# Performance work log

Hardware: AMD Instinct MI355X
Metric: run time of the kernel (lower is better)

## Reference

```python
import jax, jax.numpy as jnp
import numpy as np

B, S, D, H = 2, 2048, 1024, 16  # batch, seq, embed_dim, num_heads
DH = D // H                      # head dim = 64


def setup_inputs() -> dict:
    key = jax.random.key(0)
    kx, kq, kbq, kk, kbk, kv, kbv = jax.random.split(key, 7)
    scale = 1.0 / np.sqrt(D)
    return {
        "x": jax.random.normal(kx, (B, S, D), dtype=jnp.float32),
        "Wq": jax.random.normal(kq, (D, D), dtype=jnp.float32) * scale,
        "bq": jax.random.normal(kbq, (D,), dtype=jnp.float32) * 0.01,
        "Wk": jax.random.normal(kk, (D, D), dtype=jnp.float32) * scale,
        "bk": jax.random.normal(kbk, (D,), dtype=jnp.float32) * 0.01,
        "Wv": jax.random.normal(kv, (D, D), dtype=jnp.float32) * scale,
        "bv": jax.random.normal(kbv, (D,), dtype=jnp.float32) * 0.01,
    }


def reference(x, Wq, bq, Wk, bk, Wv, bv):
    # ooqkv_type == 'q', odeint_method == 'id': q branch = act(Linear(x)), exact GELU (torch nn.GELU default)
    q = jax.nn.gelu(x @ Wq + bq, approximate=False)
    k = x @ Wk + bk
    v = x @ Wv + bv
    # [B, S, D] -> [B, S, H, DH]
    q = q.reshape(B, S, H, DH)
    k = k.reshape(B, S, H, DH)
    v = v.reshape(B, S, H, DH)
    # NOTE: original module has NO 1/sqrt(d) scale — faithful reproduction
    att = jnp.einsum("bqhd,bkhd->bhqk", q, k)
    att = jax.nn.softmax(att, axis=-1)
    out = jnp.einsum("bhqk,bkhd->bqhd", att, v)
    return out.reshape(B, S, D)
```

## Files before the change

kernel.cpp:

```cpp
#include <hip/hip_runtime.h>
#include <math.h>

#define B_  2
#define S_  2048
#define D_  1024
#define H_  16
#define DH_ 64
#define M_  (B_ * S_)

typedef _Float16 half_t;
typedef __attribute__((ext_vector_type(8))) _Float16 h8;
typedef __attribute__((ext_vector_type(4))) _Float16 h4;
typedef __attribute__((ext_vector_type(4))) float   f32x4;

#define LOG2E 1.44269504088896f

__device__ __forceinline__ void gll16(const half_t* g, half_t* l) {
    __builtin_amdgcn_global_load_lds(
        (__attribute__((address_space(1))) const void*)g,
        (__attribute__((address_space(3))) void*)l, 16, 0, 0);
}

__global__ __launch_bounds__(256) void prep_k(
    const float* __restrict__ x, half_t* __restrict__ xh,
    const float* __restrict__ Wq, const float* __restrict__ Wk,
    const float* __restrict__ Wv, half_t* __restrict__ Wt)
{
    const int bx = blockIdx.x;
    if (bx < 2048) {
        const size_t i = ((size_t)bx * 256 + threadIdx.x) * 8;
        const float4 a = *(const float4*)(x + i);
        const float4 b = *(const float4*)(x + i + 4);
        h8 o;
        o[0] = (half_t)a.x; o[1] = (half_t)a.y; o[2] = (half_t)a.z; o[3] = (half_t)a.w;
        o[4] = (half_t)b.x; o[5] = (half_t)b.y; o[6] = (half_t)b.z; o[7] = (half_t)b.w;
        *(h8*)(xh + i) = o;
    } else {
        const int gb    = bx - 2048;
        const int which = gb >> 9;
        const float* __restrict__ W = (which == 0) ? Wq : (which == 1) ? Wk : Wv;
        half_t* __restrict__ T = Wt + (size_t)which * D_ * D_;
        const int gw   = (gb & 511) * 4 + (threadIdx.x >> 6);
        const int lane = threadIdx.x & 63;
        const int n    = (gw & 15) * 64 + lane;
        const int k0   = (gw >> 4) * 8;
        h8 o;
        #pragma unroll
        for (int t = 0; t < 8; ++t) o[t] = (half_t)W[(size_t)(k0 + t) * D_ + n];
        *(h8*)(T + (size_t)n * D_ + k0) = o;
    }
}

__global__ __launch_bounds__(256) void qkv_gemm_f16(
    const half_t* __restrict__ xh, const half_t* __restrict__ Wt,
    const float* __restrict__ bq, const float* __restrict__ bk,
    const float* __restrict__ bv,
    half_t* __restrict__ Qo, half_t* __restrict__ Ko, half_t* __restrict__ Vt)
{
    const int n0g   = blockIdx.x * 128;
    const int which = n0g >> 10;
    const int n0    = n0g & 1023;
    const int m0    = blockIdx.y * 128;
    const half_t* __restrict__ Wp  = Wt + (size_t)which * D_ * D_;
    const float* __restrict__ bias = (which == 0) ? bq : (which == 1) ? bk : bv;

    const int tid = threadIdx.x, lane = tid & 63, wave = tid >> 6;
    const int wm = (wave >> 1) * 64, wn = (wave & 1) * 64;
    const int ln = lane & 15, quad = lane >> 4;

    __shared__ __align__(16) half_t As[128 * 64];
    __shared__ __align__(16) half_t Bs[128 * 64];

    f32x4 acc[4][4];
    #pragma unroll
    for (int i = 0; i < 4; ++i)
        #pragma unroll
        for (int j = 0; j < 4; ++j) acc[i][j] = (f32x4){0.f, 0.f, 0.f, 0.f};

    for (int k0 = 0; k0 < D_; k0 += 64) {
        __syncthreads();
        #pragma unroll
        for (int l = 0; l < 4; ++l) {
            const int c  = tid + l * 256;
            const int r  = c >> 3, c0 = c & 7;
            const int cs = c0 ^ (r & 7);
            gll16(xh + (size_t)(m0 + r) * D_ + k0 + cs * 8, &As[c * 8]);
            gll16(Wp + (size_t)(n0 + r) * D_ + k0 + cs * 8, &Bs[c * 8]);
        }
        __syncthreads();

        #pragma unroll
        for (int kc = 0; kc < 2; ++kc) {
            h8 af[4], bf[4];
            #pragma unroll
            for (int i = 0; i < 4; ++i) {
                const int r = wm + i * 16 + ln;
                af[i] = *(const h8*)&As[r * 64 + (((kc << 2) + quad) ^ (r & 7)) * 8];
            }
            #pragma unroll
            for (int j = 0; j < 4; ++j) {
                const int r = wn + j * 16 + ln;
                bf[j] = *(const h8*)&Bs[r * 64 + (((kc << 2) + quad) ^ (r & 7)) * 8];
            }
            #pragma unroll
            for (int i = 0; i < 4; ++i)
                #pragma unroll
                for (int j = 0; j < 4; ++j)
                    acc[i][j] = __builtin_amdgcn_mfma_f32_16x16x32_f16(
                        af[i], bf[j], acc[i][j], 0, 0, 0);
        }
    }

    if (which == 2) {
        #pragma unroll
        for (int j = 0; j < 4; ++j) {
            const int col = n0 + wn + j * 16 + ln;
            const int h = col >> 6, d = col & 63;
            const float bb = bias[col];
            #pragma unroll
            for (int i = 0; i < 4; ++i) {
                const int sg = m0 + wm + i * 16 + quad * 4;
                const int b  = sg >> 11, srow = sg & 2047;
                h4 pv;
                #pragma unroll
                for (int r = 0; r < 4; ++r) pv[r] = (half_t)(acc[i][j][r] + bb);
                *(h4*)(Vt + (((size_t)(b * H_ + h) * DH_ + d) * S_ + srow)) = pv;
            }
        }
    } else {
        half_t* __restrict__ out = (which == 0) ? Qo : Ko;
        #pragma unroll
        for (int j = 0; j < 4; ++j) {
            const int col = n0 + wn + j * 16 + ln;
            const float bb = bias[col];
            #pragma unroll
            for (int i = 0; i < 4; ++i) {
                #pragma unroll
                for (int r = 0; r < 4; ++r) {
                    const int row = m0 + wm + i * 16 + quad * 4 + r;
                    float t = acc[i][j][r] + bb;
                    if (which == 0) {
                        const float u = t * fmaf(t * t, 0.0356774081f, 0.7978845608f);
                        const float e = __builtin_amdgcn_exp2f(u * -2.88539008178f);
                        t = t * __builtin_amdgcn_rcpf(1.0f + e) * LOG2E;
                    }
                    out[(size_t)row * D_ + col] = (half_t)t;
                }
            }
        }
    }
}

__global__ __launch_bounds__(256) void attn_f16(
    const half_t* __restrict__ Q, const half_t* __restrict__ K,
    const half_t* __restrict__ Vt, float* __restrict__ out)
{
    const int tid  = threadIdx.x;
    const int lane = tid & 63;
    const int wave = tid >> 6;
    const int ln   = lane & 15;
    const int quad = lane >> 4;
    const int bh   = blockIdx.y;
    const int b    = bh >> 4;
    const int h    = bh & 15;
    const int q0   = blockIdx.x * 128;

    const half_t* __restrict__ Qb  = Q  + (size_t)b * S_ * D_ + h * DH_;
    const half_t* __restrict__ Kb  = K  + (size_t)b * S_ * D_ + h * DH_;
    const half_t* __restrict__ Vtb = Vt + (size_t)bh * DH_ * S_;

    __shared__ __align__(16) half_t Ks[64 * 64];
    __shared__ __align__(16) half_t Vs[64 * 64];
    __shared__ __align__(16) half_t QPs[128][72];

    #pragma unroll
    for (int l = 0; l < 4; ++l) {
        const int c = tid + l * 256;
        const int r = c >> 3, k8 = c & 7;
        *(h8*)&QPs[r][k8 * 8] = *(const h8*)(Qb + (size_t)(q0 + r) * D_ + k8 * 8);
    }
    __syncthreads();
    const h8 qa0 = *(const h8*)&QPs[wave * 32 + ln][quad * 8];
    const h8 qa1 = *(const h8*)&QPs[wave * 32 + ln][32 + quad * 8];
    const h8 qc0 = *(const h8*)&QPs[wave * 32 + 16 + ln][quad * 8];
    const h8 qc1 = *(const h8*)&QPs[wave * 32 + 16 + ln][32 + quad * 8];

    h8 ones8;
    #pragma unroll
    for (int t = 0; t < 8; ++t) ones8[t] = (half_t)1.0f;

    f32x4 Oa[4], Ob[4];
    #pragma unroll
    for (int j = 0; j < 4; ++j) {
        Oa[j] = (f32x4){0.f, 0.f, 0.f, 0.f};
        Ob[j] = (f32x4){0.f, 0.f, 0.f, 0.f};
    }
    f32x4 la = (f32x4){0.f, 0.f, 0.f, 0.f};
    f32x4 lb = (f32x4){0.f, 0.f, 0.f, 0.f};
    float m_a = -INFINITY, m_b = -INFINITY;

    for (int k0 = 0; k0 < S_; k0 += 64) {
        __syncthreads();
        #pragma unroll
        for (int l = 0; l < 2; ++l) {
            const int c  = tid + l * 256;
            const int r  = c >> 3, c0 = c & 7;
            const int cs = c0 ^ (r & 7);
            gll16(Kb  + (size_t)(k0 + r) * D_ + cs * 8, &Ks[c * 8]);
            gll16(Vtb + (size_t)r * S_ + k0 + cs * 8,   &Vs[c * 8]);
        }
        __syncthreads();

        f32x4 sa[4], sb[4];
        #pragma unroll
        for (int j = 0; j < 4; ++j) {
            const int rK = j * 16 + ln;
            const h8 ka0 = *(const h8*)&Ks[rK * 64 + ((quad)     ^ (rK & 7)) * 8];
            const h8 ka1 = *(const h8*)&Ks[rK * 64 + ((quad + 4) ^ (rK & 7)) * 8];
            f32x4 t = (f32x4){0.f, 0.f, 0.f, 0.f};
            t = __builtin_amdgcn_mfma_f32_16x16x32_f16(ka0, qa0, t, 0, 0, 0);
            t = __builtin_amdgcn_mfma_f32_16x16x32_f16(ka1, qa1, t, 0, 0, 0);
            sa[j] = t;
            f32x4 u = (f32x4){0.f, 0.f, 0.f, 0.f};
            u = __builtin_amdgcn_mfma_f32_16x16x32_f16(ka0, qc0, u, 0, 0, 0);
            u = __builtin_amdgcn_mfma_f32_16x16x32_f16(ka1, qc1, u, 0, 0, 0);
            sb[j] = u;
        }

        float mxa = sa[0][0], mxb = sb[0][0];
        #pragma unroll
        for (int j = 0; j < 4; ++j)
            #pragma unroll
            for (int r = 0; r < 4; ++r) {
                mxa = fmaxf(mxa, sa[j][r]);
                mxb = fmaxf(mxb, sb[j][r]);
            }
        mxa = fmaxf(mxa, __shfl_xor(mxa, 16, 64));
        mxa = fmaxf(mxa, __shfl_xor(mxa, 32, 64));
        mxb = fmaxf(mxb, __shfl_xor(mxb, 16, 64));
        mxb = fmaxf(mxb, __shfl_xor(mxb, 32, 64));

        if (__ballot(mxa > m_a || mxb > m_b)) {
            const float mna = fmaxf(m_a, mxa);
            const float mnb = fmaxf(m_b, mxb);
            const float ala = __builtin_amdgcn_exp2f(m_a - mna);
            const float alb = __builtin_amdgcn_exp2f(m_b - mnb);
            m_a = mna; m_b = mnb;
            float ra[4], rb[4];
            #pragma unroll
            for (int r = 0; r < 4; ++r) {
                ra[r] = __shfl(ala, quad * 4 + r, 64);
                rb[r] = __shfl(alb, quad * 4 + r, 64);
            }
            #pragma unroll
            for (int r = 0; r < 4; ++r) {
                la[r] *= ra[r]; lb[r] *= rb[r];
                #pragma unroll
                for (int j = 0; j < 4; ++j) { Oa[j][r] *= ra[r]; Ob[j][r] *= rb[r]; }
            }
        }

        #pragma unroll
        for (int j = 0; j < 4; ++j) {
            h4 pva, pvb;
            #pragma unroll
            for (int r = 0; r < 4; ++r) {
                pva[r] = (half_t)__builtin_amdgcn_exp2f(sa[j][r] - m_a);
                pvb[r] = (half_t)__builtin_amdgcn_exp2f(sb[j][r] - m_b);
            }
            *(h4*)&QPs[wave * 32 + ln][j * 16 + quad * 4]      = pva;
            *(h4*)&QPs[wave * 32 + 16 + ln][j * 16 + quad * 4] = pvb;
        }

        const h8 pa0 = *(const h8*)&QPs[wave * 32 + ln][quad * 8];
        const h8 pa1 = *(const h8*)&QPs[wave * 32 + ln][32 + quad * 8];
        const h8 pb0 = *(const h8*)&QPs[wave * 32 + 16 + ln][quad * 8];
        const h8 pb1 = *(const h8*)&QPs[wave * 32 + 16 + ln][32 + quad * 8];
        #pragma unroll
        for (int j = 0; j < 4; ++j) {
            const int rV = j * 16 + ln;
            const h8 vb0 = *(const h8*)&Vs[rV * 64 + ((quad)     ^ (rV & 7)) * 8];
            const h8 vb1 = *(const h8*)&Vs[rV * 64 + ((quad + 4) ^ (rV & 7)) * 8];
            Oa[j] = __builtin_amdgcn_mfma_f32_16x16x32_f16(pa0, vb0, Oa[j], 0, 0, 0);
            Oa[j] = __builtin_amdgcn_mfma_f32_16x16x32_f16(pa1, vb1, Oa[j], 0, 0, 0);
            Ob[j] = __builtin_amdgcn_mfma_f32_16x16x32_f16(pb0, vb0, Ob[j], 0, 0, 0);
            Ob[j] = __builtin_amdgcn_mfma_f32_16x16x32_f16(pb1, vb1, Ob[j], 0, 0, 0);
        }
        la = __builtin_amdgcn_mfma_f32_16x16x32_f16(pa0, ones8, la, 0, 0, 0);
        la = __builtin_amdgcn_mfma_f32_16x16x32_f16(pa1, ones8, la, 0, 0, 0);
        lb = __builtin_amdgcn_mfma_f32_16x16x32_f16(pb0, ones8, lb, 0, 0, 0);
        lb = __builtin_amdgcn_mfma_f32_16x16x32_f16(pb1, ones8, lb, 0, 0, 0);
    }

    #pragma unroll
    for (int r = 0; r < 4; ++r) {
        const float iva = 1.0f / la[r];
        const float ivb = 1.0f / lb[r];
        const int rowa = q0 + wave * 32 + quad * 4 + r;
        const int rowb = rowa + 16;
        #pragma unroll
        for (int j = 0; j < 4; ++j) {
            out[((size_t)b * S_ + rowa) * D_ + h * DH_ + j * 16 + ln] = Oa[j][r] * iva;
            out[((size_t)b * S_ + rowb) * D_ + h * DH_ + j * 16 + ln] = Ob[j][r] * ivb;
        }
    }
}

extern "C" void kernel_launch(void* const* d_in, const int* in_sizes, int n_in,
                              void* d_out, int out_size, void* d_ws, size_t ws_size,
                              hipStream_t stream) {
    const float* x  = (const float*)d_in[0];
    const float* Wq = (const float*)d_in[1];
    const float* bq = (const float*)d_in[2];
    const float* Wk = (const float*)d_in[3];
    const float* bk = (const float*)d_in[4];
    const float* Wv = (const float*)d_in[5];
    const float* bv = (const float*)d_in[6];
    float* out = (float*)d_out;

    const size_t nmd = (size_t)M_ * D_;
    const size_t ndd = (size_t)D_ * D_;
    half_t* xh  = (half_t*)d_ws;
    half_t* Wt  = xh + nmd;
    half_t* Qh  = Wt + 3 * ndd;
    half_t* Kh  = Qh + nmd;
    half_t* Vtw = Kh + nmd;

    prep_k<<<2048 + 1536, 256, 0, stream>>>(x, xh, Wq, Wk, Wv, Wt);
    qkv_gemm_f16<<<dim3(3 * D_ / 128, M_ / 128), 256, 0, stream>>>(
        xh, Wt, bq, bk, bv, Qh, Kh, Vtw);
    attn_f16<<<dim3(S_ / 128, B_ * H_), 256, 0, stream>>>(Qh, Kh, Vtw, out);
}
```

Baseline: 197.4 us.

## Double-buffer K/V tiles in attention and raise wave priority around MFMA blocks

The attention kernel now keeps two LDS buffers each for K and V. It issues the async global-to-LDS load of the next 64-key tile before computing on the current one, so the memory transfer overlaps the QK^T, softmax and PV work. This replaces the previous two barriers per iteration with one at the end of the loop. It also wraps the MFMA sections in s_setprio to favour matrix issue. In exchange, LDS use per block roughly doubles for K/V, which may limit how many blocks fit per CU.

```diff
diff --git a/kernel.cpp b/kernel.cpp
--- a/kernel.cpp
+++ b/kernel.cpp
@@ -169,9 +169,18 @@
     const half_t* __restrict__ Kb  = K  + (size_t)b * S_ * D_ + h * DH_;
     const half_t* __restrict__ Vtb = Vt + (size_t)bh * DH_ * S_;
 
-    __shared__ __align__(16) half_t Ks[64 * 64];
-    __shared__ __align__(16) half_t Vs[64 * 64];
+    __shared__ __align__(16) half_t Ks[2][64 * 64];
+    __shared__ __align__(16) half_t Vs[2][64 * 64];
     __shared__ __align__(16) half_t QPs[128][72];
+
+    #pragma unroll
+    for (int l = 0; l < 2; ++l) {
+        const int c  = tid + l * 256;
+        const int r  = c >> 3, c0 = c & 7;
+        const int cs = c0 ^ (r & 7);
+        gll16(Kb  + (size_t)r * D_ + cs * 8, &Ks[0][c * 8]);
+        gll16(Vtb + (size_t)r * S_ + cs * 8, &Vs[0][c * 8]);
+    }
 
     #pragma unroll
     for (int l = 0; l < 4; ++l) {
@@ -199,24 +208,29 @@
     f32x4 lb = (f32x4){0.f, 0.f, 0.f, 0.f};
     float m_a = -INFINITY, m_b = -INFINITY;
 
+    int cur = 0;
     for (int k0 = 0; k0 < S_; k0 += 64) {
-        __syncthreads();
-        #pragma unroll
-        for (int l = 0; l < 2; ++l) {
-            const int c  = tid + l * 256;
-            const int r  = c >> 3, c0 = c & 7;
-            const int cs = c0 ^ (r & 7);
-            gll16(Kb  + (size_t)(k0 + r) * D_ + cs * 8, &Ks[c * 8]);
-            gll16(Vtb + (size_t)r * S_ + k0 + cs * 8,   &Vs[c * 8]);
-        }
-        __syncthreads();
-
+        if (k0 + 64 < S_) {
+            const int kn = k0 + 64;
+            #pragma unroll
+            for (int l = 0; l < 2; ++l) {
+                const int c  = tid + l * 256;
+                const int r  = c >> 3, c0 = c & 7;
+                const int cs = c0 ^ (r & 7);
+                gll16(Kb  + (size_t)(kn + r) * D_ + cs * 8, &Ks[cur ^ 1][c * 8]);
+                gll16(Vtb + (size_t)r * S_ + kn + cs * 8,   &Vs[cur ^ 1][c * 8]);
+            }
+        }
+
+        const half_t* __restrict__ Kc = Ks[cur];
+        const half_t* __restrict__ Vc = Vs[cur];
         f32x4 sa[4], sb[4];
+        __builtin_amdgcn_s_setprio(1);
         #pragma unroll
         for (int j = 0; j < 4; ++j) {
             const int rK = j * 16 + ln;
-            const h8 ka0 = *(const h8*)&Ks[rK * 64 + ((quad)     ^ (rK & 7)) * 8];
-            const h8 ka1 = *(const h8*)&Ks[rK * 64 + ((quad + 4) ^ (rK & 7)) * 8];
+            const h8 ka0 = *(const h8*)&Kc[rK * 64 + ((quad)     ^ (rK & 7)) * 8];
+            const h8 ka1 = *(const h8*)&Kc[rK * 64 + ((quad + 4) ^ (rK & 7)) * 8];
             f32x4 t = (f32x4){0.f, 0.f, 0.f, 0.f};
             t = __builtin_amdgcn_mfma_f32_16x16x32_f16(ka0, qa0, t, 0, 0, 0);
             t = __builtin_amdgcn_mfma_f32_16x16x32_f16(ka1, qa1, t, 0, 0, 0);
@@ -226,6 +240,7 @@
             u = __builtin_amdgcn_mfma_f32_16x16x32_f16(ka1, qc1, u, 0, 0, 0);
             sb[j] = u;
         }
+        __builtin_amdgcn_s_setprio(0);
 
         float mxa = sa[0][0], mxb = sb[0][0];
         #pragma unroll
@@ -276,11 +291,12 @@
         const h8 pa1 = *(const h8*)&QPs[wave * 32 + ln][32 + quad * 8];
         const h8 pb0 = *(const h8*)&QPs[wave * 32 + 16 + ln][quad * 8];
         const h8 pb1 = *(const h8*)&QPs[wave * 32 + 16 + ln][32 + quad * 8];
+        __builtin_amdgcn_s_setprio(1);
         #pragma unroll
         for (int j = 0; j < 4; ++j) {
             const int rV = j * 16 + ln;
-            const h8 vb0 = *(const h8*)&Vs[rV * 64 + ((quad)     ^ (rV & 7)) * 8];
-            const h8 vb1 = *(const h8*)&Vs[rV * 64 + ((quad + 4) ^ (rV & 7)) * 8];
+            const h8 vb0 = *(const h8*)&Vc[rV * 64 + ((quad)     ^ (rV & 7)) * 8];
+            const h8 vb1 = *(const h8*)&Vc[rV * 64 + ((quad + 4) ^ (rV & 7)) * 8];
             Oa[j] = __builtin_amdgcn_mfma_f32_16x16x32_f16(pa0, vb0, Oa[j], 0, 0, 0);
             Oa[j] = __builtin_amdgcn_mfma_f32_16x16x32_f16(pa1, vb1, Oa[j], 0, 0, 0);
             Ob[j] = __builtin_amdgcn_mfma_f32_16x16x32_f16(pb0, vb0, Ob[j], 0, 0, 0);
@@ -290,6 +306,10 @@
         la = __builtin_amdgcn_mfma_f32_16x16x32_f16(pa1, ones8, la, 0, 0, 0);
         lb = __builtin_amdgcn_mfma_f32_16x16x32_f16(pb0, ones8, lb, 0, 0, 0);
         lb = __builtin_amdgcn_mfma_f32_16x16x32_f16(pb1, ones8, lb, 0, 0, 0);
+        __builtin_amdgcn_s_setprio(0);
+
+        __syncthreads();
+        cur ^= 1;
     }
 
     #pragma unroll
```

Result: no change. 197.3 us (-0.0%).

## Split attention block into 8 waves of 16 query rows each

Applied to the files above, without the earlier changes.

The attention kernel moves from 4 waves each handling 32 query rows to 8 waves each handling 16 rows, so a 512-thread block covers the same 128 queries. Each thread now issues a single K and V async load per tile, using precomputed source pointers that advance by pointer increment. s_setprio hints are wrapped around the MFMA sections. The aim is more wave-level parallelism and latency hiding, at the cost of K/V LDS fragments being re-read by twice as many waves and less register-level reuse per wave.

```diff
diff --git a/kernel.cpp b/kernel.cpp
--- a/kernel.cpp
+++ b/kernel.cpp
@@ -151,7 +151,7 @@
     }
 }
 
-__global__ __launch_bounds__(256) void attn_f16(
+__global__ __launch_bounds__(512) void attn_f16(
     const half_t* __restrict__ Q, const half_t* __restrict__ K,
     const half_t* __restrict__ Vt, float* __restrict__ out)
 {
@@ -173,45 +173,45 @@
     __shared__ __align__(16) half_t Vs[64 * 64];
     __shared__ __align__(16) half_t QPs[128][72];
 
-    #pragma unroll
-    for (int l = 0; l < 4; ++l) {
-        const int c = tid + l * 256;
+    {
+    }
+    const int sr  = tid >> 3, sc0 = tid & 7;
+    const int scs = sc0 ^ (sr & 7);
+    const half_t* kSrc = Kb  + (size_t)sr * D_ + scs * 8;
+    const half_t* vSrc = Vtb + (size_t)sr * S_ + scs * 8;
+    half_t* const kDst = &Ks[tid * 8];
+    half_t* const vDst = &Vs[tid * 8];
+
+    #pragma unroll
+    for (int l = 0; l < 2; ++l) {
+        const int c = tid + l * 512;
         const int r = c >> 3, k8 = c & 7;
         *(h8*)&QPs[r][k8 * 8] = *(const h8*)(Qb + (size_t)(q0 + r) * D_ + k8 * 8);
     }
     __syncthreads();
-    const h8 qa0 = *(const h8*)&QPs[wave * 32 + ln][quad * 8];
-    const h8 qa1 = *(const h8*)&QPs[wave * 32 + ln][32 + quad * 8];
-    const h8 qc0 = *(const h8*)&QPs[wave * 32 + 16 + ln][quad * 8];
-    const h8 qc1 = *(const h8*)&QPs[wave * 32 + 16 + ln][32 + quad * 8];
+    const h8 qa0 = *(const h8*)&QPs[wave * 16 + ln][quad * 8];
+    const h8 qa1 = *(const h8*)&QPs[wave * 16 + ln][32 + quad * 8];
 
     h8 ones8;
     #pragma unroll
     for (int t = 0; t < 8; ++t) ones8[t] = (half_t)1.0f;
 
-    f32x4 Oa[4], Ob[4];
-    #pragma unroll
-    for (int j = 0; j < 4; ++j) {
-        Oa[j] = (f32x4){0.f, 0.f, 0.f, 0.f};
-        Ob[j] = (f32x4){0.f, 0.f, 0.f, 0.f};
-    }
+    f32x4 Oa[4];
+    #pragma unroll
+    for (int j = 0; j < 4; ++j) Oa[j] = (f32x4){0.f, 0.f, 0.f, 0.f};
     f32x4 la = (f32x4){0.f, 0.f, 0.f, 0.f};
-    f32x4 lb = (f32x4){0.f, 0.f, 0.f, 0.f};
-    float m_a = -INFINITY, m_b = -INFINITY;
+    float m_a = -INFINITY;
 
     for (int k0 = 0; k0 < S_; k0 += 64) {
         __syncthreads();
-        #pragma unroll
-        for (int l = 0; l < 2; ++l) {
-            const int c  = tid + l * 256;
-            const int r  = c >> 3, c0 = c & 7;
-            const int cs = c0 ^ (r & 7);
-            gll16(Kb  + (size_t)(k0 + r) * D_ + cs * 8, &Ks[c * 8]);
-            gll16(Vtb + (size_t)r * S_ + k0 + cs * 8,   &Vs[c * 8]);
-        }
+        gll16(kSrc, kDst);
+        gll16(vSrc, vDst);
+        kSrc += 64 * D_;
+        vSrc += 64;
         __syncthreads();
 
-        f32x4 sa[4], sb[4];
+        f32x4 sa[4];
+        __builtin_amdgcn_s_setprio(1);
         #pragma unroll
         for (int j = 0; j < 4; ++j) {
             const int rK = j * 16 + ln;
@@ -221,61 +221,44 @@
             t = __builtin_amdgcn_mfma_f32_16x16x32_f16(ka0, qa0, t, 0, 0, 0);
             t = __builtin_amdgcn_mfma_f32_16x16x32_f16(ka1, qa1, t, 0, 0, 0);
             sa[j] = t;
-            f32x4 u = (f32x4){0.f, 0.f, 0.f, 0.f};
-            u = __builtin_amdgcn_mfma_f32_16x16x32_f16(ka0, qc0, u, 0, 0, 0);
-            u = __builtin_amdgcn_mfma_f32_16x16x32_f16(ka1, qc1, u, 0, 0, 0);
-            sb[j] = u;
-        }
-
-        float mxa = sa[0][0], mxb = sb[0][0];
+        }
+        __builtin_amdgcn_s_setprio(0);
+
+        float mxa = sa[0][0];
         #pragma unroll
         for (int j = 0; j < 4; ++j)
             #pragma unroll
-            for (int r = 0; r < 4; ++r) {
-                mxa = fmaxf(mxa, sa[j][r]);
-                mxb = fmaxf(mxb, sb[j][r]);
-            }
+            for (int r = 0; r < 4; ++r) mxa = fmaxf(mxa, sa[j][r]);
         mxa = fmaxf(mxa, __shfl_xor(mxa, 16, 64));
         mxa = fmaxf(mxa, __shfl_xor(mxa, 32, 64));
-        mxb = fmaxf(mxb, __shfl_xor(mxb, 16, 64));
-        mxb = fmaxf(mxb, __shfl_xor(mxb, 32, 64));
-
-        if (__ballot(mxa > m_a || mxb > m_b)) {
+
+        if (__ballot(mxa > m_a)) {
             const float mna = fmaxf(m_a, mxa);
-            const float mnb = fmaxf(m_b, mxb);
             const float ala = __builtin_amdgcn_exp2f(m_a - mna);
-            const float alb = __builtin_amdgcn_exp2f(m_b - mnb);
-            m_a = mna; m_b = mnb;
-            float ra[4], rb[4];
+            m_a = mna;
+            float ra[4];
+            #pragma unroll
+            for (int r = 0; r < 4; ++r) ra[r] = __shfl(ala, quad * 4 + r, 64);
             #pragma unroll
             for (int r = 0; r < 4; ++r) {
-                ra[r] = __shfl(ala, quad * 4 + r, 64);
-                rb[r] = __shfl(alb, quad * 4 + r, 64);
-            }
-            #pragma unroll
-            for (int r = 0; r < 4; ++r) {
-                la[r] *= ra[r]; lb[r] *= rb[r];
+                la[r] *= ra[r];
                 #pragma unroll
-                for (int j = 0; j < 4; ++j) { Oa[j][r] *= ra[r]; Ob[j][r] *= rb[r]; }
-            }
-        }
-
-        #pragma unroll
-        for (int j = 0; j < 4; ++j) {
-            h4 pva, pvb;
-            #pragma unroll
-            for (int r = 0; r < 4; ++r) {
+                for (int j = 0; j < 4; ++j) Oa[j][r] *= ra[r];
+            }
+        }
+
+        #pragma unroll
+        for (int j = 0; j < 4; ++j) {
+            h4 pva;
+            #pragma unroll
+            for (int r = 0; r < 4; ++r)
                 pva[r] = (half_t)__builtin_amdgcn_exp2f(sa[j][r] - m_a);
-                pvb[r] = (half_t)__builtin_amdgcn_exp2f(sb[j][r] - m_b);
-            }
-            *(h4*)&QPs[wave * 32 + ln][j * 16 + quad * 4]      = pva;
-            *(h4*)&QPs[wave * 32 + 16 + ln][j * 16 + quad * 4] = pvb;
-        }
-
-        const h8 pa0 = *(const h8*)&QPs[wave * 32 + ln][quad * 8];
-        const h8 pa1 = *(const h8*)&QPs[wave * 32 + ln][32 + quad * 8];
-        const h8 pb0 = *(const h8*)&QPs[wave * 32 + 16 + ln][quad * 8];
-        const h8 pb1 = *(const h8*)&QPs[wave * 32 + 16 + ln][32 + quad * 8];
+            *(h4*)&QPs[wave * 16 + ln][j * 16 + quad * 4] = pva;
+        }
+
+        const h8 pa0 = *(const h8*)&QPs[wave * 16 + ln][quad * 8];
+        const h8 pa1 = *(const h8*)&QPs[wave * 16 + ln][32 + quad * 8];
+        __builtin_amdgcn_s_setprio(1);
         #pragma unroll
         for (int j = 0; j < 4; ++j) {
             const int rV = j * 16 + ln;
@@ -283,26 +266,19 @@
             const h8 vb1 = *(const h8*)&Vs[rV * 64 + ((quad + 4) ^ (rV & 7)) * 8];
             Oa[j] = __builtin_amdgcn_mfma_f32_16x16x32_f16(pa0, vb0, Oa[j], 0, 0, 0);
             Oa[j] = __builtin_amdgcn_mfma_f32_16x16x32_f16(pa1, vb1, Oa[j], 0, 0, 0);
-            Ob[j] = __builtin_amdgcn_mfma_f32_16x16x32_f16(pb0, vb0, Ob[j], 0, 0, 0);
-            Ob[j] = __builtin_amdgcn_mfma_f32_16x16x32_f16(pb1, vb1, Ob[j], 0, 0, 0);
         }
         la = __builtin_amdgcn_mfma_f32_16x16x32_f16(pa0, ones8, la, 0, 0, 0);
         la = __builtin_amdgcn_mfma_f32_16x16x32_f16(pa1, ones8, la, 0, 0, 0);
-        lb = __builtin_amdgcn_mfma_f32_16x16x32_f16(pb0, ones8, lb, 0, 0, 0);
-        lb = __builtin_amdgcn_mfma_f32_16x16x32_f16(pb1, ones8, lb, 0, 0, 0);
+        __builtin_amdgcn_s_setprio(0);
     }
 
     #pragma unroll
     for (int r = 0; r < 4; ++r) {
         const float iva = 1.0f / la[r];
-        const float ivb = 1.0f / lb[r];
-        const int rowa = q0 + wave * 32 + quad * 4 + r;
-        const int rowb = rowa + 16;
-        #pragma unroll
-        for (int j = 0; j < 4; ++j) {
+        const int rowa = q0 + wave * 16 + quad * 4 + r;
+        #pragma unroll
+        for (int j = 0; j < 4; ++j)
             out[((size_t)b * S_ + rowa) * D_ + h * DH_ + j * 16 + ln] = Oa[j][r] * iva;
-            out[((size_t)b * S_ + rowb) * D_ + h * DH_ + j * 16 + ln] = Ob[j][r] * ivb;
-        }
     }
 }
 
@@ -329,5 +305,5 @@
     prep_k<<<2048 + 1536, 256, 0, stream>>>(x, xh, Wq, Wk, Wv, Wt);
     qkv_gemm_f16<<<dim3(3 * D_ / 128, M_ / 128), 256, 0, stream>>>(
         xh, Wt, bq, bk, bv, Qh, Kh, Vtw);
-    attn_f16<<<dim3(S_ / 128, B_ * H_), 256, 0, stream>>>(Qh, Kh, Vtw, out);
-}
+    attn_f16<<<dim3(S_ / 128, B_ * H_), 512, 0, stream>>>(Qh, Kh, Vtw, out);
+}
```

New measurement: 186.5 us. -5.5%, faster.
